# Optimization experiments

Hardware: AMD Instinct MI355X
Metric: run time of the kernel (lower is better)

The kernel has to match this reference:

```python
import jax, jax.numpy as jnp
import numpy as np

NUM_EMBEDDINGS = 1024
EMBEDDING_DIM = 256


def setup_inputs() -> dict:
    key = jax.random.key(0)
    k1, k2 = jax.random.split(key)
    x = jax.random.normal(k1, (32, 256, 32, 32), dtype=jnp.float32)
    # nn.Embedding initialized uniform(-1/K, 1/K)
    bound = 1.0 / NUM_EMBEDDINGS
    weight = jax.random.uniform(k2, (NUM_EMBEDDINGS, EMBEDDING_DIM),
                                dtype=jnp.float32, minval=-bound, maxval=bound)
    return {"x": x, "weight": weight}


def reference(x, weight):
    # _preprocess: [B, C, H, W] -> [B, H, W, C] -> [B*H*W, C]
    B, C, H, W = x.shape
    encoded_flat = jnp.transpose(x, (0, 2, 3, 1)).reshape(-1, C)  # [N, D]

    # squared euclidean distances (cdist(...)**2): ||e||^2 - 2 e.w + ||w||^2
    dists = (jnp.sum(encoded_flat * encoded_flat, axis=1, keepdims=True)
             - 2.0 * (encoded_flat @ weight.T)
             + jnp.sum(weight * weight, axis=1))  # [N, K]
    codebook_indices = jnp.argmin(dists, axis=1)  # [N] int

    quantized_flat = weight[codebook_indices]  # [N, D] gather
    # straight-through estimator
    quantized_flat = encoded_flat + jax.lax.stop_gradient(quantized_flat - encoded_flat)

    # _postprocess: [N, D] -> [B, H, W, C] -> [B, C, H, W]
    quantized = jnp.transpose(quantized_flat.reshape(B, H, W, C), (0, 3, 1, 2))
    return encoded_flat, quantized_flat, codebook_indices, quantized
```

## Files before the change

kernel.cpp:

```cpp
#include <hip/hip_runtime.h>

#define K_CODES 1024
#define DIM 256
#define N_TOT 32768
#define LCAP 192

typedef _Float16 f16;
typedef _Float16 f16x8 __attribute__((ext_vector_type(8)));
typedef float f32x4 __attribute__((ext_vector_type(4)));

__device__ __forceinline__ float np_pw128_sq(const float* __restrict__ v) {
    float r[8];
    #pragma unroll
    for (int j = 0; j < 8; ++j) r[j] = __fmul_rn(v[j], v[j]);
    #pragma unroll
    for (int i = 1; i < 16; ++i)
        #pragma unroll
        for (int j = 0; j < 8; ++j)
            r[j] = __fadd_rn(r[j], __fmul_rn(v[8*i+j], v[8*i+j]));
    const float t01 = __fadd_rn(r[0], r[1]);
    const float t23 = __fadd_rn(r[2], r[3]);
    const float t45 = __fadd_rn(r[4], r[5]);
    const float t67 = __fadd_rn(r[6], r[7]);
    return __fadd_rn(__fadd_rn(t01, t23), __fadd_rn(t45, t67));
}

__global__ void vq_wnorm_kernel(const float* __restrict__ weight, float* __restrict__ wnorm) {
    int k = blockIdx.x * blockDim.x + threadIdx.x;
    if (k >= K_CODES) return;
    const float* wr = weight + (size_t)k * DIM;
    wnorm[k] = __fadd_rn(np_pw128_sq(wr), np_pw128_sq(wr + 128));
}

__global__ __launch_bounds__(64) void vq_convw_kernel(
    const float* __restrict__ weight, f16* __restrict__ Whs)
{
    const int t = threadIdx.x;
    const int code = blockIdx.x * 2 + (t >> 5);
    const int unit = t & 31;
    const float4 v0 = *(const float4*)&weight[(size_t)code * DIM + unit * 8];
    const float4 v1 = *(const float4*)&weight[(size_t)code * DIM + unit * 8 + 4];
    f16x8 o;
    o[0]=(f16)(v0.x*1024.f); o[1]=(f16)(v0.y*1024.f); o[2]=(f16)(v0.z*1024.f); o[3]=(f16)(v0.w*1024.f);
    o[4]=(f16)(v1.x*1024.f); o[5]=(f16)(v1.y*1024.f); o[6]=(f16)(v1.z*1024.f); o[7]=(f16)(v1.w*1024.f);
    const int du = unit ^ (code & 7);
    *(f16x8*)&Whs[(size_t)code * DIM + du * 8] = o;
}

template<bool PRE>
__global__ __launch_bounds__(256) __attribute__((amdgpu_waves_per_eu(4)))
void vq_fused_kernel(
    const float* __restrict__ x, const float* __restrict__ weight,
    const float* __restrict__ wnorm, const f16* __restrict__ Whs,
    float* __restrict__ enc_out, float* __restrict__ idx_out)
{
    __shared__ __align__(16) char WlRaw[33280];
    __shared__ float wn[K_CODES];
    __shared__ unsigned rm[32];
    __shared__ unsigned long long rmEx[32];
    __shared__ unsigned list[LCAP];
    __shared__ unsigned lcount;

    char* const Wb = WlRaw;
    float (*F)[260] = (float(*)[260])WlRaw;

    const int tid = threadIdx.x;
    const int blk = blockIdx.x;
    const int b = blk >> 5, h = blk & 31;
    const long n0 = (long)blk * 32;
    const int wid = tid >> 6, lane = tid & 63;
    const int qw = wid;
    const int fr = lane & 15, fg = lane >> 4;

    if (tid < 32) { rm[tid] = 0xFFFFFFFFu; rmEx[tid] = 0xFFFFFFFFFFFFFFFFull; }
    if (tid == 0) lcount = 0;
    #pragma unroll
    for (int i = 0; i < 4; ++i) wn[tid + i * 256] = wnorm[tid + i * 256];

    {
        const int wq = tid & 7, cb = tid >> 3;
        for (int c = cb; c < DIM; c += 32) {
            const float4 v = *(const float4*)&x[(((long)b * DIM + c) * 32 + h) * 32 + wq * 4];
            F[wq * 4 + 0][c] = v.x; F[wq * 4 + 1][c] = v.y;
            F[wq * 4 + 2][c] = v.z; F[wq * 4 + 3][c] = v.w;
        }
    }
    __syncthreads();
    {
        const int c4 = tid & 63, rg = tid >> 6;
        #pragma unroll
        for (int r0 = 0; r0 < 32; r0 += 4) {
            const int row = r0 + rg;
            *(float4*)&enc_out[(n0 + row) * DIM + c4 * 4] = *(const float4*)&F[row][c4 * 4];
        }
    }
    f16x8 afr[2][8];
    #pragma unroll
    for (int mt = 0; mt < 2; ++mt)
        #pragma unroll
        for (int kk = 0; kk < 8; ++kk) {
            const float4 lo = *(const float4*)&F[mt * 16 + fr][kk * 32 + fg * 8];
            const float4 hi = *(const float4*)&F[mt * 16 + fr][kk * 32 + fg * 8 + 4];
            f16x8 a;
            a[0] = (f16)lo.x; a[1] = (f16)lo.y; a[2] = (f16)lo.z; a[3] = (f16)lo.w;
            a[4] = (f16)hi.x; a[5] = (f16)hi.y; a[6] = (f16)hi.z; a[7] = (f16)hi.w;
            afr[mt][kk] = a;
        }
    __syncthreads();

    unsigned s1[8], s2[8];
    #pragma unroll
    for (int i = 0; i < 8; ++i) { s1[i] = 0xFFFFFFFFu; s2[i] = 0xFFFFFFFFu; }

    for (int ch = 0; ch < 16; ++ch) {
        if (PRE) {
            const char* src = (const char*)Whs + (size_t)ch * 32768 + wid * 1024 + lane * 16;
            #pragma unroll
            for (int u = 0; u < 8; ++u) {
                __builtin_amdgcn_global_load_lds(
                    (const __attribute__((address_space(1))) void*)(src + u * 4096),
                    (__attribute__((address_space(3))) void*)(Wb + (u * 4 + wid) * 1024), 16, 0, 0);
            }
        } else {
            #pragma unroll
            for (int u = 0; u < 8; ++u) {
                const int flat = u * 256 + tid;
                const int code = flat >> 5, unit = flat & 31;
                const float4 v0 = *(const float4*)&weight[(long)(ch * 64 + code) * DIM + unit * 8];
                const float4 v1 = *(const float4*)&weight[(long)(ch * 64 + code) * DIM + unit * 8 + 4];
                f16x8 t;
                t[0]=(f16)(v0.x*1024.f); t[1]=(f16)(v0.y*1024.f); t[2]=(f16)(v0.z*1024.f); t[3]=(f16)(v0.w*1024.f);
                t[4]=(f16)(v1.x*1024.f); t[5]=(f16)(v1.y*1024.f); t[6]=(f16)(v1.z*1024.f); t[7]=(f16)(v1.w*1024.f);
                *(f16x8*)(Wb + code * 512 + (unit ^ (code & 7)) * 16) = t;
            }
        }
        __syncthreads();

        const int cl = qw * 16 + fr;
        const int code = ch * 64 + cl;
        f32x4 acc0 = {0.f, 0.f, 0.f, 0.f}, acc1 = {0.f, 0.f, 0.f, 0.f};
        #pragma unroll
        for (int kk = 0; kk < 8; ++kk) {
            const f16x8 bfr = *(const f16x8*)(Wb + cl * 512 + (((kk * 4 + fg) ^ (fr & 7)) * 16));
            acc0 = __builtin_amdgcn_mfma_f32_16x16x32_f16(afr[0][kk], bfr, acc0, 0, 0, 0);
            acc1 = __builtin_amdgcn_mfma_f32_16x16x32_f16(afr[1][kk], bfr, acc1, 0, 0, 0);
        }
        const float wnk = wn[code];
        #pragma unroll
        for (int q = 0; q < 4; ++q) {
            {
                const float vp = fmaf(acc0[q], -0.001953125f, wnk);
                const unsigned uq = (unsigned)fmaf(vp, 1048576.0f, 1048576.0f);
                const unsigned u = uq * 1024u + (unsigned)code;
                s2[q] = min(s2[q], max(s1[q], u));
                s1[q] = min(s1[q], u);
            }
            {
                const float vp = fmaf(acc1[q], -0.001953125f, wnk);
                const unsigned uq = (unsigned)fmaf(vp, 1048576.0f, 1048576.0f);
                const unsigned u = uq * 1024u + (unsigned)code;
                s2[4 + q] = min(s2[4 + q], max(s1[4 + q], u));
                s1[4 + q] = min(s1[4 + q], u);
            }
        }
        __syncthreads();
    }

    #pragma unroll
    for (int sl = 0; sl < 8; ++sl) {
        unsigned bmin = s1[sl];
        bmin = min(bmin, (unsigned)__shfl_xor((int)bmin, 1));
        bmin = min(bmin, (unsigned)__shfl_xor((int)bmin, 2));
        bmin = min(bmin, (unsigned)__shfl_xor((int)bmin, 4));
        bmin = min(bmin, (unsigned)__shfl_xor((int)bmin, 8));
        if (fr == 0) {
            const int row = (sl >> 2) * 16 + fg * 4 + (sl & 3);
            atomicMin(&rm[row], bmin);
        }
    }
    __syncthreads();

    auto exact_check = [&](int row, int k) {
        const float* ep = enc_out + (n0 + row) * DIM;
        const float* wp = weight + (long)k * DIM;
        float dot = 0.0f;
        float rr[8];
        #pragma unroll
        for (int j = 0; j < 8; ++j) rr[j] = 0.0f;
        #pragma unroll
        for (int dp = 0; dp < 16; ++dp) {
            {
                const float4 ev = *(const float4*)&ep[dp * 8];
                const float4 wv = *(const float4*)&wp[dp * 8];
                dot = __fmaf_rn(ev.x, wv.x, dot); dot = __fmaf_rn(ev.y, wv.y, dot);
                dot = __fmaf_rn(ev.z, wv.z, dot); dot = __fmaf_rn(ev.w, wv.w, dot);
                rr[0] = __fadd_rn(rr[0], __fmul_rn(ev.x, ev.x));
                rr[1] = __fadd_rn(rr[1], __fmul_rn(ev.y, ev.y));
                rr[2] = __fadd_rn(rr[2], __fmul_rn(ev.z, ev.z));
                rr[3] = __fadd_rn(rr[3], __fmul_rn(ev.w, ev.w));
            }
            {
                const float4 ev = *(const float4*)&ep[dp * 8 + 4];
                const float4 wv = *(const float4*)&wp[dp * 8 + 4];
                dot = __fmaf_rn(ev.x, wv.x, dot); dot = __fmaf_rn(ev.y, wv.y, dot);
                dot = __fmaf_rn(ev.z, wv.z, dot); dot = __fmaf_rn(ev.w, wv.w, dot);
                rr[4] = __fadd_rn(rr[4], __fmul_rn(ev.x, ev.x));
                rr[5] = __fadd_rn(rr[5], __fmul_rn(ev.y, ev.y));
                rr[6] = __fadd_rn(rr[6], __fmul_rn(ev.z, ev.z));
                rr[7] = __fadd_rn(rr[7], __fmul_rn(ev.w, ev.w));
            }
        }
        const float bA = __fadd_rn(__fadd_rn(__fadd_rn(rr[0], rr[1]), __fadd_rn(rr[2], rr[3])),
                                   __fadd_rn(__fadd_rn(rr[4], rr[5]), __fadd_rn(rr[6], rr[7])));
        #pragma unroll
        for (int j = 0; j < 8; ++j) rr[j] = 0.0f;
        #pragma unroll
        for (int dp = 0; dp < 16; ++dp) {
            {
                const float4 ev = *(const float4*)&ep[128 + dp * 8];
                const float4 wv = *(const float4*)&wp[128 + dp * 8];
                dot = __fmaf_rn(ev.x, wv.x, dot); dot = __fmaf_rn(ev.y, wv.y, dot);
                dot = __fmaf_rn(ev.z, wv.z, dot); dot = __fmaf_rn(ev.w, wv.w, dot);
                rr[0] = __fadd_rn(rr[0], __fmul_rn(ev.x, ev.x));
                rr[1] = __fadd_rn(rr[1], __fmul_rn(ev.y, ev.y));
                rr[2] = __fadd_rn(rr[2], __fmul_rn(ev.z, ev.z));
                rr[3] = __fadd_rn(rr[3], __fmul_rn(ev.w, ev.w));
            }
            {
                const float4 ev = *(const float4*)&ep[128 + dp * 8 + 4];
                const float4 wv = *(const float4*)&wp[128 + dp * 8 + 4];
                dot = __fmaf_rn(ev.x, wv.x, dot); dot = __fmaf_rn(ev.y, wv.y, dot);
                dot = __fmaf_rn(ev.z, wv.z, dot); dot = __fmaf_rn(ev.w, wv.w, dot);
                rr[4] = __fadd_rn(rr[4], __fmul_rn(ev.x, ev.x));
                rr[5] = __fadd_rn(rr[5], __fmul_rn(ev.y, ev.y));
                rr[6] = __fadd_rn(rr[6], __fmul_rn(ev.z, ev.z));
                rr[7] = __fadd_rn(rr[7], __fmul_rn(ev.w, ev.w));
            }
        }
        const float bB = __fadd_rn(__fadd_rn(__fadd_rn(rr[0], rr[1]), __fadd_rn(rr[2], rr[3])),
                                   __fadd_rn(__fadd_rn(rr[4], rr[5]), __fadd_rn(rr[6], rr[7])));
        const float sEr = __fadd_rn(bA, bB);
        const float vex = __fadd_rn(__fadd_rn(sEr, -__fmul_rn(2.0f, dot)), wn[k]);
        const unsigned long long pk =
            (((unsigned long long)__float_as_uint(vex)) << 10) | (unsigned long long)k;
        atomicMin(&rmEx[row], pk);
    };

    #pragma unroll
    for (int sl = 0; sl < 8; ++sl) {
        const int row = (sl >> 2) * 16 + fg * 4 + (sl & 3);
        const unsigned thr = (rm[row] >> 10) + 1000u;
        #pragma unroll
        for (int c = 0; c < 2; ++c) {
            const unsigned u = c ? s2[sl] : s1[sl];
            if ((u >> 10) <= thr) {
                const unsigned pos = atomicAdd(&lcount, 1u);
                if (pos < LCAP) list[pos] = ((unsigned)row << 10) | (u & 1023u);
                else exact_check(row, (int)(u & 1023u));
            }
        }
    }
    __syncthreads();
    {
        const unsigned cnt = min(lcount, (unsigned)LCAP);
        for (unsigned t = tid; t < cnt; t += 256) {
            const unsigned ent = list[t];
            exact_check((int)(ent >> 10), (int)(ent & 1023u));
        }
    }
    __syncthreads();

    if (tid < 32) idx_out[n0 + tid] = (float)(unsigned)(rmEx[tid] & 1023ull);
}

__global__ __launch_bounds__(256) void vq_gather_kernel(
    const float* __restrict__ weight, const float* __restrict__ idx_in,
    float* __restrict__ qf_out, float* __restrict__ q_out)
{
    __shared__ __align__(16) float F[32][260];
    __shared__ int kk[32];
    const int tid = threadIdx.x;
    const int blk = blockIdx.x;
    const int b = blk >> 5, h = blk & 31;
    const long n0 = (long)blk * 32;

    if (tid < 32) kk[tid] = (int)idx_in[n0 + tid];
    __syncthreads();
    {
        const int c4 = tid & 63, rg = tid >> 6;
        #pragma unroll
        for (int r0 = 0; r0 < 32; r0 += 4) {
            const int row = r0 + rg;
            const int k = kk[row];
            const float4 v = *(const float4*)&weight[(long)k * DIM + c4 * 4];
            *(float4*)&qf_out[(n0 + row) * DIM + c4 * 4] = v;
            *(float4*)&F[row][c4 * 4] = v;
        }
    }
    __syncthreads();
    {
        const int w = tid & 31, c0 = tid >> 5;
        for (int c = c0; c < DIM; c += 8)
            q_out[(((long)b * DIM + c) * 32 + h) * 32 + w] = F[w][c];
    }
}

extern "C" void kernel_launch(void* const* d_in, const int* in_sizes, int n_in,
                              void* d_out, int out_size, void* d_ws, size_t ws_size,
                              hipStream_t stream)
{
    const float* x      = (const float*)d_in[0];
    const float* weight = (const float*)d_in[1];

    float* out = (float*)d_out;
    float* enc = out;
    float* qf  = enc + (size_t)N_TOT * DIM;
    float* idx = qf  + (size_t)N_TOT * DIM;
    float* qo  = idx + N_TOT;

    float* wnorm = (float*)d_ws;
    f16*   Whs   = (f16*)((char*)d_ws + 4096);

    const bool pre = ws_size >= (size_t)(4096 + K_CODES * DIM * 2 + 64);

    vq_wnorm_kernel<<<K_CODES / 256, 256, 0, stream>>>(weight, wnorm);
    if (pre) {
        vq_convw_kernel<<<K_CODES / 2, 64, 0, stream>>>(weight, Whs);
        vq_fused_kernel<true><<<1024, 256, 0, stream>>>(x, weight, wnorm, Whs, enc, idx);
    } else {
        vq_fused_kernel<false><<<1024, 256, 0, stream>>>(x, weight, wnorm, Whs, enc, idx);
    }
    vq_gather_kernel<<<1024, 256, 0, stream>>>(weight, idx, qf, qo);
}
```

Baseline: 80.96 us.

## Load codebook fragments directly from global memory instead of staging through LDS

The f16 codebook is now stored transposed by 8-element unit so each lane's MFMA B fragment is a contiguous 16-byte global load. The fused kernel drops the per-chunk LDS staging and both __syncthreads per chunk, and each wave handles its own 256 codes. This removes block-wide barriers and LDS traffic, but every block now reads the full codebook from global/L2 with no sharing across waves. The ws_size check and the non-precomputed fallback are gone, and an unused declaration was added.

```diff
diff --git a/kernel.cpp b/kernel.cpp
--- a/kernel.cpp
+++ b/kernel.cpp
@@ -32,37 +32,32 @@
     wnorm[k] = __fadd_rn(np_pw128_sq(wr), np_pw128_sq(wr + 128));
 }
 
-__global__ __launch_bounds__(64) void vq_convw_kernel(
-    const float* __restrict__ weight, f16* __restrict__ Whs)
+__global__ __launch_bounds__(256) void vq_convw_kernel(
+    const float* __restrict__ weight, f16* __restrict__ Wht)
 {
-    const int t = threadIdx.x;
-    const int code = blockIdx.x * 2 + (t >> 5);
-    const int unit = t & 31;
+    const int g = blockIdx.x * 256 + threadIdx.x;
+    const int unit = g >> 10, code = g & 1023;
     const float4 v0 = *(const float4*)&weight[(size_t)code * DIM + unit * 8];
     const float4 v1 = *(const float4*)&weight[(size_t)code * DIM + unit * 8 + 4];
     f16x8 o;
     o[0]=(f16)(v0.x*1024.f); o[1]=(f16)(v0.y*1024.f); o[2]=(f16)(v0.z*1024.f); o[3]=(f16)(v0.w*1024.f);
     o[4]=(f16)(v1.x*1024.f); o[5]=(f16)(v1.y*1024.f); o[6]=(f16)(v1.z*1024.f); o[7]=(f16)(v1.w*1024.f);
-    const int du = unit ^ (code & 7);
-    *(f16x8*)&Whs[(size_t)code * DIM + du * 8] = o;
+    *(f16x8*)&Wht[((size_t)unit * 1024 + code) * 8] = o;
 }
 
 template<bool PRE>
 __global__ __launch_bounds__(256) __attribute__((amdgpu_waves_per_eu(4)))
 void vq_fused_kernel(
     const float* __restrict__ x, const float* __restrict__ weight,
-    const float* __restrict__ wnorm, const f16* __restrict__ Whs,
+    const float* __restrict__ wnorm, const f16* __restrict__ Wht,
     float* __restrict__ enc_out, float* __restrict__ idx_out)
 {
-    __shared__ __align__(16) char WlRaw[33280];
+    __shared__ __align__(16) float F[32][260];
     __shared__ float wn[K_CODES];
     __shared__ unsigned rm[32];
     __shared__ unsigned long long rmEx[32];
     __shared__ unsigned list[LCAP];
     __shared__ unsigned lcount;
-
-    char* const Wb = WlRaw;
-    float (*F)[260] = (float(*)[260])WlRaw;
 
     const int tid = threadIdx.x;
     const int blk = blockIdx.x;
@@ -112,38 +107,21 @@
     #pragma unroll
     for (int i = 0; i < 8; ++i) { s1[i] = 0xFFFFFFFFu; s2[i] = 0xFFFFFFFFu; }
 
-    for (int ch = 0; ch < 16; ++ch) {
-        if (PRE) {
-            const char* src = (const char*)Whs + (size_t)ch * 32768 + wid * 1024 + lane * 16;
-            #pragma unroll
-            for (int u = 0; u < 8; ++u) {
-                __builtin_amdgcn_global_load_lds(
-                    (const __attribute__((address_space(1))) void*)(src + u * 4096),
-                    (__attribute__((address_space(3))) void*)(Wb + (u * 4 + wid) * 1024), 16, 0, 0);
-            }
-        } else {
-            #pragma unroll
-            for (int u = 0; u < 8; ++u) {
-                const int flat = u * 256 + tid;
-                const int code = flat >> 5, unit = flat & 31;
-                const float4 v0 = *(const float4*)&weight[(long)(ch * 64 + code) * DIM + unit * 8];
-                const float4 v1 = *(const float4*)&weight[(long)(ch * 64 + code) * DIM + unit * 8 + 4];
-                f16x8 t;
-                t[0]=(f16)(v0.x*1024.f); t[1]=(f16)(v0.y*1024.f); t[2]=(f16)(v0.z*1024.f); t[3]=(f16)(v0.w*1024.f);
-                t[4]=(f16)(v1.x*1024.f); t[5]=(f16)(v1.y*1024.f); t[6]=(f16)(v1.z*1024.f); t[7]=(f16)(v1.w*1024.f);
-                *(f16x8*)(Wb + code * 512 + (unit ^ (code & 7)) * 16) = t;
-            }
-        }
-        __syncthreads();
-
-        const int cl = qw * 16 + fr;
-        const int code = ch * 64 + cl;
+    const int lane_code = qw * 256 + fr;
+    const f16* const wbase = Wht + ((size_t)fg * 1024 + lane_code) * 8;
+
+    #pragma unroll 2
+    for (int ct = 0; ct < 16; ++ct) {
+        const int code = qw * 256 + ct * 16 + fr;
         f32x4 acc0 = {0.f, 0.f, 0.f, 0.f}, acc1 = {0.f, 0.f, 0.f, 0.f};
+        f16x8 bfr[8];
+        #pragma unroll
+        for (int kk = 0; kk < 8; ++kk)
+            bfr[kk] = *(const f16x8*)(wbase + ((size_t)kk * 4096 + ct * 16) * 8);
         #pragma unroll
         for (int kk = 0; kk < 8; ++kk) {
-            const f16x8 bfr = *(const f16x8*)(Wb + cl * 512 + (((kk * 4 + fg) ^ (fr & 7)) * 16));
-            acc0 = __builtin_amdgcn_mfma_f32_16x16x32_f16(afr[0][kk], bfr, acc0, 0, 0, 0);
-            acc1 = __builtin_amdgcn_mfma_f32_16x16x32_f16(afr[1][kk], bfr, acc1, 0, 0, 0);
+            acc0 = __builtin_amdgcn_mfma_f32_16x16x32_f16(afr[0][kk], bfr[kk], acc0, 0, 0, 0);
+            acc1 = __builtin_amdgcn_mfma_f32_16x16x32_f16(afr[1][kk], bfr[kk], acc1, 0, 0, 0);
         }
         const float wnk = wn[code];
         #pragma unroll
@@ -163,7 +141,6 @@
                 s1[4 + q] = min(s1[4 + q], u);
             }
         }
-        __syncthreads();
     }
 
     #pragma unroll
@@ -272,6 +249,12 @@
 
     if (tid < 32) idx_out[n0 + tid] = (float)(unsigned)(rmEx[tid] & 1023ull);
 }
+
+__global__ __launch_bounds__(256) __attribute__((amdgpu_waves_per_eu(4)))
+void vq_fused_nopre(
+    const float* __restrict__ x, const float* __restrict__ weight,
+    const float* __restrict__ wnorm,
+    float* __restrict__ enc_out, float* __restrict__ idx_out);
 
 __global__ __launch_bounds__(256) void vq_gather_kernel(
     const float* __restrict__ weight, const float* __restrict__ idx_in,
@@ -319,16 +302,10 @@
     float* qo  = idx + N_TOT;
 
     float* wnorm = (float*)d_ws;
-    f16*   Whs   = (f16*)((char*)d_ws + 4096);
-
-    const bool pre = ws_size >= (size_t)(4096 + K_CODES * DIM * 2 + 64);
+    f16*   Wht   = (f16*)((char*)d_ws + 4096);
 
     vq_wnorm_kernel<<<K_CODES / 256, 256, 0, stream>>>(weight, wnorm);
-    if (pre) {
-        vq_convw_kernel<<<K_CODES / 2, 64, 0, stream>>>(weight, Whs);
-        vq_fused_kernel<true><<<1024, 256, 0, stream>>>(x, weight, wnorm, Whs, enc, idx);
-    } else {
-        vq_fused_kernel<false><<<1024, 256, 0, stream>>>(x, weight, wnorm, Whs, enc, idx);
-    }
+    vq_convw_kernel<<<128, 256, 0, stream>>>(weight, Wht);
+    vq_fused_kernel<true><<<1024, 256, 0, stream>>>(x, weight, wnorm, Wht, enc, idx);
     vq_gather_kernel<<<1024, 256, 0, stream>>>(weight, idx, qf, qo);
 }
```

Result: faster. 77.08 us (-4.8%).
